# Optimization experiments

Measured on AMD Instinct MI355X. Metric: run time of the kernel, lower is better.

Reference implementation:

```python
import jax, jax.numpy as jnp
import numpy as np

N_NODES = 50000
N_EDGES = 800000
IN_F = 128
OUT_F = 128
HEADS = 4
HEAD_DIM = OUT_F // HEADS


def setup_inputs() -> dict:
    key = jax.random.key(0)
    ks = jax.random.split(key, 10)
    x = jax.random.normal(ks[0], (N_NODES, IN_F), dtype=jnp.float32)
    edge_index = jax.random.randint(ks[1], (2, N_EDGES), 0, N_NODES)
    sc = 0.05
    wq = jax.random.normal(ks[2], (HEADS, IN_F, HEAD_DIM), dtype=jnp.float32) * sc
    bq = jax.random.normal(ks[3], (HEADS, HEAD_DIM), dtype=jnp.float32) * sc
    wk = jax.random.normal(ks[4], (HEADS, IN_F, HEAD_DIM), dtype=jnp.float32) * sc
    bk = jax.random.normal(ks[5], (HEADS, HEAD_DIM), dtype=jnp.float32) * sc
    wv = jax.random.normal(ks[6], (HEADS, IN_F, HEAD_DIM), dtype=jnp.float32) * sc
    bv = jax.random.normal(ks[7], (HEADS, HEAD_DIM), dtype=jnp.float32) * sc
    wo = jax.random.normal(ks[8], (OUT_F, OUT_F), dtype=jnp.float32) * sc
    bo = jax.random.normal(ks[9], (OUT_F,), dtype=jnp.float32) * sc
    return {"x": x, "edge_index": edge_index, "wq": wq, "bq": bq,
            "wk": wk, "bk": bk, "wv": wv, "bv": bv, "wo": wo, "bo": bo}


def reference(x, edge_index, wq, bq, wk, bk, wv, bv, wo, bo):
    n = x.shape[0]
    src, tgt = edge_index[0], edge_index[1]
    # per-head linear projections: [H, N, hd]
    q = jnp.einsum('nf,hfd->hnd', x, wq) + bq[:, None, :]
    k = jnp.einsum('nf,hfd->hnd', x, wk) + bk[:, None, :]
    v = jnp.einsum('nf,hfd->hnd', x, wv) + bv[:, None, :]
    # per-edge scores: dot(q[target], k[source]) -> [H, E]
    scores = jnp.einsum('hed,hed->he', q[:, tgt], k[:, src])

    def seg_softmax(s):  # s: [E], softmax over edges sharing the same target
        m = jax.ops.segment_max(s, tgt, num_segments=n)  # [N] (-inf for isolated)
        e = jnp.exp(s - m[tgt])
        den = jax.ops.segment_sum(e, tgt, num_segments=n)
        return e / den[tgt]

    alpha = jax.vmap(seg_softmax)(scores)  # [H, E]

    def aggregate(a, vh):  # a: [E], vh: [N, hd]
        return jax.ops.segment_sum(a[:, None] * vh[src], tgt, num_segments=n)

    agg = jax.vmap(aggregate)(alpha, v)  # [H, N, hd]; isolated nodes -> zeros
    out = agg.transpose(1, 0, 2).reshape(n, HEADS * HEAD_DIM)  # concat heads
    return out @ wo.T + bo
```

## Files before the change

kernel.cpp:

```cpp
#include <hip/hip_runtime.h>
#include <math.h>

#define F 128
#define HEADS 4
#define HD 32

typedef unsigned short ushort_t;
typedef unsigned int uint_t;

__device__ __forceinline__ ushort_t f2bf(float f) {
    uint_t u = __float_as_uint(f);
    u += 0x7FFFu + ((u >> 16) & 1u);
    return (ushort_t)(u >> 16);
}
__device__ __forceinline__ float bf2f(ushort_t h) {
    return __uint_as_float(((uint_t)h) << 16);
}

__global__ void hist_kernel(const int* __restrict__ tgt, int* __restrict__ cnt, int E) {
    int i = blockIdx.x * blockDim.x + threadIdx.x;
    if (i < E) atomicAdd(&cnt[tgt[i]], 1);
}

__global__ void scan_part1(const int* __restrict__ cnt, int* __restrict__ bsum, int N) {
    __shared__ int ws[4];
    int t = threadIdx.x;
    int base = blockIdx.x * 1024;
    int s = 0;
#pragma unroll
    for (int r = 0; r < 4; r++) {
        int i = base + t + 256 * r;
        if (i < N) s += cnt[i];
    }
    for (int d = 1; d < 64; d <<= 1) s += __shfl_xor(s, d);
    if ((t & 63) == 0) ws[t >> 6] = s;
    __syncthreads();
    if (t == 0) bsum[blockIdx.x] = ws[0] + ws[1] + ws[2] + ws[3];
}

__global__ void scan_part2(const int* __restrict__ bsum, int* __restrict__ boff,
                           int* __restrict__ row_off, int NB, int N) {
    int t = threadIdx.x;
    int v = (t < NB) ? bsum[t] : 0;
    int incl = v;
    for (int d = 1; d < 64; d <<= 1) {
        int n = __shfl_up(incl, d);
        if (t >= d) incl += n;
    }
    if (t < NB) boff[t] = incl - v;
    if (t == 63) row_off[N] = incl;
}

__global__ void scan_part3(const int* __restrict__ cnt, const int* __restrict__ boff,
                           int* __restrict__ row_off, int* __restrict__ next_, int N) {
    __shared__ int wsum[4];
    int t = threadIdx.x, lane = t & 63, wid = t >> 6;
    int base = blockIdx.x * 1024;
    int i0 = base + t * 4;
    int e0 = (i0 + 0 < N) ? cnt[i0 + 0] : 0;
    int e1 = (i0 + 1 < N) ? cnt[i0 + 1] : 0;
    int e2 = (i0 + 2 < N) ? cnt[i0 + 2] : 0;
    int e3 = (i0 + 3 < N) ? cnt[i0 + 3] : 0;
    int p0 = e0, p1 = p0 + e1, p2 = p1 + e2, p3 = p2 + e3;
    int incl = p3;
    for (int d = 1; d < 64; d <<= 1) {
        int n = __shfl_up(incl, d);
        if (lane >= d) incl += n;
    }
    int texcl = incl - p3;
    if (lane == 63) wsum[wid] = incl;
    __syncthreads();
    if (t == 0) {
        int a = wsum[0];
        int b = a + wsum[1];
        int c = b + wsum[2];
        wsum[1] = a; wsum[2] = b; wsum[3] = c; wsum[0] = 0;
    }
    __syncthreads();
    int off = boff[blockIdx.x] + wsum[wid] + texcl;
    if (i0 + 0 < N) { row_off[i0 + 0] = off;      next_[i0 + 0] = off; }
    if (i0 + 1 < N) { row_off[i0 + 1] = off + p0; next_[i0 + 1] = off + p0; }
    if (i0 + 2 < N) { row_off[i0 + 2] = off + p1; next_[i0 + 2] = off + p1; }
    if (i0 + 3 < N) { row_off[i0 + 3] = off + p2; next_[i0 + 3] = off + p2; }
}

__global__ void scatter_kernel(const int* __restrict__ src, const int* __restrict__ tgt,
                               int* __restrict__ next_, int* __restrict__ csr_src, int E) {
    int i = blockIdx.x * blockDim.x + threadIdx.x;
    if (i < E) {
        int tg = tgt[i];
        int pos = atomicAdd(&next_[tg], 1);
        csr_src[pos] = src[i];
    }
}

__device__ __forceinline__ void store4(float* p, float4 v) { *(float4*)p = v; }
__device__ __forceinline__ void store4(ushort_t* p, float4 v) {
    ushort4 h;
    h.x = f2bf(v.x); h.y = f2bf(v.y); h.z = f2bf(v.z); h.w = f2bf(v.w);
    *(ushort4*)p = h;
}

template<typename OT>
__device__ __forceinline__ void gemm_body(const float* __restrict__ x, const float* __restrict__ b,
                                          OT* __restrict__ out, int N,
                                          const float* Wl, float* Xl) {
    int t = threadIdx.x;
    int c4 = t & 31;
    int nl = t >> 5;
    float4 bb = *(const float4*)&b[4 * c4];
    for (int nb = blockIdx.x * 32; nb < N; nb += gridDim.x * 32) {
#pragma unroll
        for (int r = 0; r < 4; r++) {
            int idx = t + 256 * r;
            int node = idx >> 5, f4 = idx & 31;
            int gn = nb + node;
            float4 xv = (gn < N) ? *(const float4*)&x[(size_t)gn * F + 4 * f4]
                                 : make_float4(0.f, 0.f, 0.f, 0.f);
            *(float4*)&Xl[node * F + 4 * f4] = xv;
        }
        __syncthreads();
        float4 acc[4];
#pragma unroll
        for (int j = 0; j < 4; j++) acc[j] = bb;
#pragma unroll 2
        for (int f = 0; f < 128; f += 4) {
            float4 w0 = *(const float4*)&Wl[(f + 0) * F + 4 * c4];
            float4 w1 = *(const float4*)&Wl[(f + 1) * F + 4 * c4];
            float4 w2 = *(const float4*)&Wl[(f + 2) * F + 4 * c4];
            float4 w3 = *(const float4*)&Wl[(f + 3) * F + 4 * c4];
#pragma unroll
            for (int j = 0; j < 4; j++) {
                float4 xv = *(const float4*)&Xl[(nl + 8 * j) * F + f];
                acc[j].x += xv.x * w0.x + xv.y * w1.x + xv.z * w2.x + xv.w * w3.x;
                acc[j].y += xv.x * w0.y + xv.y * w1.y + xv.z * w2.y + xv.w * w3.y;
                acc[j].z += xv.x * w0.z + xv.y * w1.z + xv.z * w2.z + xv.w * w3.z;
                acc[j].w += xv.x * w0.w + xv.y * w1.w + xv.z * w2.w + xv.w * w3.w;
            }
        }
#pragma unroll
        for (int j = 0; j < 4; j++) {
            int gn = nb + nl + 8 * j;
            if (gn < N) store4(&out[(size_t)gn * F + 4 * c4], acc[j]);
        }
        __syncthreads();
    }
}

__global__ __launch_bounds__(256, 2) void proj_q_kernel(
    const float* __restrict__ x, const float* __restrict__ wq, const float* __restrict__ bq,
    float* __restrict__ qo, int N) {
    __shared__ float Wl[128 * 128];
    __shared__ float Xl[32 * 128];
    int t = threadIdx.x;
    int c4 = t & 31, h = c4 >> 3, d4 = c4 & 7;
    const float4* w4 = (const float4*)wq;
#pragma unroll
    for (int r = 0; r < 16; r++) {
        int f = (t >> 5) + 8 * r;
        *(float4*)&Wl[f * F + 4 * c4] = w4[h * 1024 + f * 8 + d4];
    }
    __syncthreads();
    gemm_body<float>(x, bq, qo, N, Wl, Xl);
}

__global__ __launch_bounds__(256, 2) void proj_kv_kernel(
    const float* __restrict__ x,
    const float* __restrict__ wk, const float* __restrict__ bk,
    const float* __restrict__ wv, const float* __restrict__ bv,
    ushort_t* __restrict__ ko, ushort_t* __restrict__ vo, int N) {
    __shared__ float Wl[128 * 128];
    __shared__ float Xl[32 * 128];
    const float* w = blockIdx.y == 0 ? wk : wv;
    const float* b = blockIdx.y == 0 ? bk : bv;
    ushort_t* out = blockIdx.y == 0 ? ko : vo;
    int t = threadIdx.x;
    int c4 = t & 31, h = c4 >> 3, d4 = c4 & 7;
    const float4* w4 = (const float4*)w;
#pragma unroll
    for (int r = 0; r < 16; r++) {
        int f = (t >> 5) + 8 * r;
        *(float4*)&Wl[f * F + 4 * c4] = w4[h * 1024 + f * 8 + d4];
    }
    __syncthreads();
    gemm_body<ushort_t>(x, b, out, N, Wl, Xl);
}

__global__ __launch_bounds__(256, 2) void outproj_kernel(
    const float* __restrict__ aggin, const float* __restrict__ wo,
    const float* __restrict__ bo, float* __restrict__ out, int N) {
    __shared__ float Wl[128 * 128];
    __shared__ float Xl[32 * 128];
    int t = threadIdx.x;
    int c4 = t & 31;
#pragma unroll
    for (int r = 0; r < 16; r++) {
        int f = (t >> 5) + 8 * r;
        float4 wv4;
        wv4.x = wo[(size_t)(4 * c4 + 0) * F + f];
        wv4.y = wo[(size_t)(4 * c4 + 1) * F + f];
        wv4.z = wo[(size_t)(4 * c4 + 2) * F + f];
        wv4.w = wo[(size_t)(4 * c4 + 3) * F + f];
        *(float4*)&Wl[f * F + 4 * c4] = wv4;
    }
    __syncthreads();
    gemm_body<float>(aggin, bo, out, N, Wl, Xl);
}

__global__ __launch_bounds__(256) void edge_attn_kernel(
    const float* __restrict__ q, const ushort_t* __restrict__ kb,
    const ushort_t* __restrict__ vb,
    const int* __restrict__ row_off, const int* __restrict__ csr_src,
    float* __restrict__ agg, int N) {
    int wave = (blockIdx.x * blockDim.x + threadIdx.x) >> 6;
    if (wave >= N) return;
    int lane = threadIdx.x & 63;
    int n = wave;
    int h4 = lane & 3;
    int slot = lane >> 2;
    int hagg = lane >> 4;

    float4 qf[8];
#pragma unroll
    for (int i = 0; i < 8; i++)
        qf[i] = *(const float4*)&q[(size_t)n * F + i * 16 + h4 * 4];

    int base = row_off[n];
    int deg = row_off[n + 1] - base;

    float m_sc = -INFINITY;
    float m_ag = -INFINITY;
    float den = 0.f;
    float2 accA = make_float2(0.f, 0.f);
    float2 accB = make_float2(0.f, 0.f);

    for (int c0 = 0; c0 < deg; c0 += 16) {
        int rem = deg - c0;
        int nj = rem < 16 ? rem : 16;
        int mye = c0 + slot;
        int srcn = (mye < deg) ? csr_src[base + mye] : 0;

        float sacc[4] = {0.f, 0.f, 0.f, 0.f};
#pragma unroll
        for (int i = 0; i < 8; i++) {
            ushort4 kk = *(const ushort4*)&kb[(size_t)srcn * F + i * 16 + h4 * 4];
            sacc[i >> 1] += qf[i].x * bf2f(kk.x) + qf[i].y * bf2f(kk.y)
                          + qf[i].z * bf2f(kk.z) + qf[i].w * bf2f(kk.w);
        }
#pragma unroll
        for (int hh = 0; hh < 4; hh++) {
            sacc[hh] += __shfl_xor(sacc[hh], 1);
            sacc[hh] += __shfl_xor(sacc[hh], 2);
        }
        float s = h4 == 0 ? sacc[0] : h4 == 1 ? sacc[1] : h4 == 2 ? sacc[2] : sacc[3];
        if (mye >= deg) s = -INFINITY;

        float cm = s;
        cm = fmaxf(cm, __shfl_xor(cm, 4));
        cm = fmaxf(cm, __shfl_xor(cm, 8));
        cm = fmaxf(cm, __shfl_xor(cm, 16));
        cm = fmaxf(cm, __shfl_xor(cm, 32));

        float nm_sc = fmaxf(m_sc, cm);
        float cm_ag = __shfl(cm, hagg);
        float nm_ag = fmaxf(m_ag, cm_ag);

        float p = __expf(s - nm_sc);
        float psum = p;
        psum += __shfl_xor(psum, 4);
        psum += __shfl_xor(psum, 8);
        psum += __shfl_xor(psum, 16);
        psum += __shfl_xor(psum, 32);

        float scale = __expf(m_ag - nm_ag);
        den = den * scale + __shfl(psum, hagg);
        accA.x *= scale; accA.y *= scale;
        accB.x *= scale; accB.y *= scale;

#pragma unroll 4
        for (int j = 0; j < nj; j++) {
            float pj = __shfl(p, (j << 2) | hagg);
            int sj = __shfl(srcn, j << 2);
            uint_t vv = *(const uint_t*)&vb[(size_t)sj * F + lane * 2];
            float v0 = bf2f((ushort_t)(vv & 0xFFFFu));
            float v1 = bf2f((ushort_t)(vv >> 16));
            if (j & 1) { accB.x += pj * v0; accB.y += pj * v1; }
            else       { accA.x += pj * v0; accA.y += pj * v1; }
        }
        m_sc = nm_sc;
        m_ag = nm_ag;
    }
    float inv = (den > 0.f) ? 1.f / den : 0.f;
    *(float2*)&agg[(size_t)n * F + lane * 2] =
        make_float2((accA.x + accB.x) * inv, (accA.y + accB.y) * inv);
}

extern "C" void kernel_launch(void* const* d_in, const int* in_sizes, int n_in,
                              void* d_out, int out_size, void* d_ws, size_t ws_size,
                              hipStream_t stream) {
    const float* x  = (const float*)d_in[0];
    const int*   ei = (const int*)d_in[1];
    const float* wq = (const float*)d_in[2];
    const float* bq = (const float*)d_in[3];
    const float* wk = (const float*)d_in[4];
    const float* bk = (const float*)d_in[5];
    const float* wv = (const float*)d_in[6];
    const float* bv = (const float*)d_in[7];
    const float* wo = (const float*)d_in[8];
    const float* bo = (const float*)d_in[9];
    float* out = (float*)d_out;

    int N = in_sizes[0] / F;
    int E = in_sizes[1] / 2;
    const int* srcs = ei;
    const int* tgts = ei + E;

    size_t need = (size_t)N * F * 4 * 2
                + (size_t)N * F * 2 * 2
                + (size_t)(N + 1) * 4
                + (size_t)N * 4 * 2
                + (size_t)E * 4
                + 128 * 4;
    if (ws_size < need) return;

    char* wsp = (char*)d_ws;
    float* q       = (float*)wsp;    wsp += (size_t)N * F * 4;
    float* agg     = (float*)wsp;    wsp += (size_t)N * F * 4;
    ushort_t* kb   = (ushort_t*)wsp; wsp += (size_t)N * F * 2;
    ushort_t* vb   = (ushort_t*)wsp; wsp += (size_t)N * F * 2;
    int* row_off = (int*)wsp; wsp += (size_t)(N + 1) * 4;
    int* next_   = (int*)wsp; wsp += (size_t)N * 4;
    int* cnt     = (int*)wsp; wsp += (size_t)N * 4;
    int* csr_src = (int*)wsp; wsp += (size_t)E * 4;
    int* bsum    = (int*)wsp; wsp += 64 * 4;
    int* boff    = (int*)wsp; wsp += 64 * 4;

    int NB = (N + 1023) >> 10;

    hipMemsetAsync(cnt, 0, (size_t)N * 4, stream);
    hist_kernel<<<(E + 255) / 256, 256, 0, stream>>>(tgts, cnt, E);
    scan_part1<<<NB, 256, 0, stream>>>(cnt, bsum, N);
    scan_part2<<<1, 64, 0, stream>>>(bsum, boff, row_off, NB, N);
    scan_part3<<<NB, 256, 0, stream>>>(cnt, boff, row_off, next_, N);
    scatter_kernel<<<(E + 255) / 256, 256, 0, stream>>>(srcs, tgts, next_, csr_src, E);
    proj_q_kernel<<<512, 256, 0, stream>>>(x, wq, bq, q, N);
    proj_kv_kernel<<<dim3(512, 2), 256, 0, stream>>>(x, wk, bk, wv, bv, kb, vb, N);
    edge_attn_kernel<<<(N + 3) / 4, 256, 0, stream>>>(q, kb, vb, row_off, csr_src, agg, N);
    outproj_kernel<<<512, 256, 0, stream>>>(agg, wo, bo, out, N);
}
```

Measured before the change: 418.4 us.

## Split wave into four edge groups with 16-byte V loads in aggregation

After: 377.9 us. 1.11x faster.

```diff
diff --git a/kernel.cpp b/kernel.cpp
--- a/kernel.cpp
+++ b/kernel.cpp
@@ -218,7 +218,9 @@
     int n = wave;
     int h4 = lane & 3;
     int slot = lane >> 2;
-    int hagg = lane >> 4;
+    int li = lane & 15;
+    int g = lane >> 4;
+    int hag = li >> 2;
 
     float4 qf[8];
 #pragma unroll
@@ -231,12 +233,9 @@
     float m_sc = -INFINITY;
     float m_ag = -INFINITY;
     float den = 0.f;
-    float2 accA = make_float2(0.f, 0.f);
-    float2 accB = make_float2(0.f, 0.f);
+    float acc[8] = {0.f, 0.f, 0.f, 0.f, 0.f, 0.f, 0.f, 0.f};
 
     for (int c0 = 0; c0 < deg; c0 += 16) {
-        int rem = deg - c0;
-        int nj = rem < 16 ? rem : 16;
         int mye = c0 + slot;
         int srcn = (mye < deg) ? csr_src[base + mye] : 0;
 
@@ -262,7 +261,7 @@
         cm = fmaxf(cm, __shfl_xor(cm, 32));
 
         float nm_sc = fmaxf(m_sc, cm);
-        float cm_ag = __shfl(cm, hagg);
+        float cm_ag = __shfl(cm, hag);
         float nm_ag = fmaxf(m_ag, cm_ag);
 
         float p = __expf(s - nm_sc);
@@ -273,26 +272,40 @@
         psum += __shfl_xor(psum, 32);
 
         float scale = __expf(m_ag - nm_ag);
-        den = den * scale + __shfl(psum, hagg);
-        accA.x *= scale; accA.y *= scale;
-        accB.x *= scale; accB.y *= scale;
-
-#pragma unroll 4
-        for (int j = 0; j < nj; j++) {
-            float pj = __shfl(p, (j << 2) | hagg);
-            int sj = __shfl(srcn, j << 2);
-            uint_t vv = *(const uint_t*)&vb[(size_t)sj * F + lane * 2];
-            float v0 = bf2f((ushort_t)(vv & 0xFFFFu));
-            float v1 = bf2f((ushort_t)(vv >> 16));
-            if (j & 1) { accB.x += pj * v0; accB.y += pj * v1; }
-            else       { accA.x += pj * v0; accA.y += pj * v1; }
+        den = den * scale + __shfl(psum, hag);
+#pragma unroll
+        for (int d = 0; d < 8; d++) acc[d] *= scale;
+
+#pragma unroll
+        for (int r = 0; r < 4; r++) {
+            int e = (r << 2) | g;
+            float pj = __shfl(p, (e << 2) | hag);
+            int sj = __shfl(srcn, e << 2);
+            uint4 vv = *(const uint4*)&vb[(size_t)sj * F + li * 8];
+            acc[0] += pj * bf2f((ushort_t)(vv.x & 0xFFFFu));
+            acc[1] += pj * bf2f((ushort_t)(vv.x >> 16));
+            acc[2] += pj * bf2f((ushort_t)(vv.y & 0xFFFFu));
+            acc[3] += pj * bf2f((ushort_t)(vv.y >> 16));
+            acc[4] += pj * bf2f((ushort_t)(vv.z & 0xFFFFu));
+            acc[5] += pj * bf2f((ushort_t)(vv.z >> 16));
+            acc[6] += pj * bf2f((ushort_t)(vv.w & 0xFFFFu));
+            acc[7] += pj * bf2f((ushort_t)(vv.w >> 16));
         }
         m_sc = nm_sc;
         m_ag = nm_ag;
     }
+#pragma unroll
+    for (int d = 0; d < 8; d++) {
+        acc[d] += __shfl_xor(acc[d], 16);
+        acc[d] += __shfl_xor(acc[d], 32);
+    }
     float inv = (den > 0.f) ? 1.f / den : 0.f;
-    *(float2*)&agg[(size_t)n * F + lane * 2] =
-        make_float2((accA.x + accB.x) * inv, (accA.y + accB.y) * inv);
+    if (g == 0) {
+        float4 o0 = make_float4(acc[0] * inv, acc[1] * inv, acc[2] * inv, acc[3] * inv);
+        float4 o1 = make_float4(acc[4] * inv, acc[5] * inv, acc[6] * inv, acc[7] * inv);
+        *(float4*)&agg[(size_t)n * F + li * 8] = o0;
+        *(float4*)&agg[(size_t)n * F + li * 8 + 4] = o1;
+    }
 }
 
 extern "C" void kernel_launch(void* const* d_in, const int* in_sizes, int n_in,
```
